# Kernel tuning notes

Hardware: AMD Instinct MI355X
Metric: run time of the kernel (lower is better)

Reference implementation:

```python
import jax, jax.numpy as jnp
import numpy as np

N, E, FDIM, HID, HEADS, C, L, G = 50000, 800000, 512, 256, 8, 32, 3, 64
EPS = 1e-5


def setup_inputs() -> dict:
    key = jax.random.key(0)
    ks = jax.random.split(key, 16)
    x = jax.random.normal(ks[0], (N, FDIM), dtype=jnp.float32)
    edge_index = jax.random.randint(ks[1], (2, E), 0, N, dtype=jnp.int32)
    batch = jnp.sort(jax.random.randint(ks[2], (N,), 0, G, dtype=jnp.int32))
    s = lambda f: 1.0 / np.sqrt(f)
    return {
        "x": x,
        "edge_index": edge_index,
        "batch": batch,
        "in_w": jax.random.normal(ks[3], (FDIM, HID), jnp.float32) * s(FDIM),
        "in_b": jnp.zeros((HID,), jnp.float32),
        "gat_w": jax.random.normal(ks[4], (L, HID, HID), jnp.float32) * s(HID),
        "att_src": jax.random.normal(ks[5], (L, HEADS, C), jnp.float32) * s(C),
        "att_dst": jax.random.normal(ks[6], (L, HEADS, C), jnp.float32) * s(C),
        "gat_b": jnp.zeros((L, HID), jnp.float32),
        "res_w": jax.random.normal(ks[7], (L, HID, HID), jnp.float32) * s(HID),
        "res_b": jnp.zeros((L, HID), jnp.float32),
        "ln_g": jnp.ones((L, HID), jnp.float32),
        "ln_b": jnp.zeros((L, HID), jnp.float32),
        "pool_w": jax.random.normal(ks[8], (2 * HID, HID), jnp.float32) * s(2 * HID),
        "pool_b": jnp.zeros((HID,), jnp.float32),
    }


def _gat_layer(h, src, dst, w, a_src, a_dst, b):
    # PyG GATConv, concat=True, negative_slope=0.2, dropout inactive (eval)
    xh = (h @ w).reshape(N, HEADS, C)                      # [N,H,C]
    asn = jnp.einsum('nhc,hc->nh', xh, a_src)              # [N,H]
    adn = jnp.einsum('nhc,hc->nh', xh, a_dst)
    e = jax.nn.leaky_relu(asn[src] + adn[dst], 0.2)        # [E2,H]
    # scatter-softmax over destination neighborhoods
    m = jax.ops.segment_max(e, dst, num_segments=N)
    m = jnp.where(jnp.isfinite(m), m, 0.0)
    ex = jnp.exp(e - m[dst])
    den = jax.ops.segment_sum(ex, dst, num_segments=N)
    alpha = ex / (den[dst] + 1e-16)                        # [E2,H]
    msg = xh[src] * alpha[:, :, None]                      # [E2,H,C]
    out = jax.ops.segment_sum(msg, dst, num_segments=N)    # [N,H,C]
    return out.reshape(N, HID) + b


def _layer_norm(h, g, b):
    mu = jnp.mean(h, axis=-1, keepdims=True)
    var = jnp.mean((h - mu) ** 2, axis=-1, keepdims=True)
    return (h - mu) * jax.lax.rsqrt(var + EPS) * g + b


def reference(x, edge_index, batch, in_w, in_b, gat_w, att_src, att_dst, gat_b,
              res_w, res_b, ln_g, ln_b, pool_w, pool_b):
    loops = jnp.arange(N, dtype=edge_index.dtype)          # GATConv add_self_loops=True
    src = jnp.concatenate([edge_index[0], loops])
    dst = jnp.concatenate([edge_index[1], loops])
    h = x @ in_w + in_b
    for i in range(L):
        h_res = h @ res_w[i] + res_b[i]
        h = _gat_layer(h, src, dst, gat_w[i], att_src[i], att_dst[i], gat_b[i])
        h = jax.nn.relu(_layer_norm(h + h_res, ln_g[i], ln_b[i]))
    ones = jnp.ones((N,), h.dtype)
    cnt = jax.ops.segment_sum(ones, batch, num_segments=G)
    h_mean = jax.ops.segment_sum(h, batch, num_segments=G) / jnp.maximum(cnt, 1.0)[:, None]
    h_max = jax.ops.segment_max(h, batch, num_segments=G)
    h_cat = jnp.concatenate([h_mean, h_max], axis=1)       # [G, 2*HID]
    return jax.nn.relu(h_cat @ pool_w + pool_b)            # [G, HID]
```

## Files before the change

kernel.cpp:

```cpp
#include <hip/hip_runtime.h>
#include <math.h>

#define N_NODES 50000
#define E_EDGES 800000
#define E2 (E_EDGES + N_NODES)
#define M_PAD 50048
#define FDIM 512
#define HID 256
#define HEADS 8
#define CDIM 32
#define LAYERS 3
#define GRAPHS 64
#define LN_EPS 1e-5f
#define POOL_P 16

typedef unsigned short ushort_t;
typedef __attribute__((ext_vector_type(8))) short short8v;
typedef __attribute__((ext_vector_type(4))) float f32x4;

__device__ __forceinline__ float bf2f(ushort_t u) {
    union { unsigned int i; float f; } v;
    v.i = ((unsigned int)u) << 16;
    return v.f;
}
__device__ __forceinline__ ushort_t f2bf(float f) {
    union { float f; unsigned int u; } v;
    v.f = f;
    unsigned int r = (v.u + 0x7FFFu + ((v.u >> 16) & 1u)) >> 16;
    return (ushort_t)r;
}
__device__ __forceinline__ void gload_lds16(const void* g, void* l) {
    __builtin_amdgcn_global_load_lds(
        (const __attribute__((address_space(1))) void*)g,
        (__attribute__((address_space(3))) void*)l, 16, 0, 0);
}

__global__ void k_count(const int* __restrict__ ei, int* __restrict__ cnt) {
    int e = blockIdx.x * 256 + threadIdx.x;
    if (e >= E2) return;
    int dst = (e < E_EDGES) ? ei[E_EDGES + e] : (e - E_EDGES);
    atomicAdd(&cnt[dst], 1);
}

__global__ void k_scan1(const int* __restrict__ cnt, int* __restrict__ part) {
    __shared__ int s[256];
    int t = threadIdx.x;
    int i = blockIdx.x * 256 + t;
    s[t] = (i < N_NODES) ? cnt[i] : 0;
    __syncthreads();
    for (int d = 128; d > 0; d >>= 1) {
        if (t < d) s[t] += s[t + d];
        __syncthreads();
    }
    if (t == 0) part[blockIdx.x] = s[0];
}

__global__ void k_scan2(int* __restrict__ part, int nb, int* __restrict__ rowptr) {
    __shared__ int s[256];
    int t = threadIdx.x;
    int v = (t < nb) ? part[t] : 0;
    s[t] = v;
    __syncthreads();
    for (int d = 1; d < 256; d <<= 1) {
        int x = (t >= d) ? s[t - d] : 0;
        __syncthreads();
        s[t] += x;
        __syncthreads();
    }
    if (t < nb) part[t] = s[t] - v;
    if (t == 255) rowptr[N_NODES] = s[255];
}

__global__ void k_scan3(const int* __restrict__ cnt, const int* __restrict__ part,
                        int* __restrict__ rowptr) {
    __shared__ int s[256];
    int t = threadIdx.x;
    int i = blockIdx.x * 256 + t;
    int v = (i < N_NODES) ? cnt[i] : 0;
    s[t] = v;
    __syncthreads();
    for (int d = 1; d < 256; d <<= 1) {
        int x = (t >= d) ? s[t - d] : 0;
        __syncthreads();
        s[t] += x;
        __syncthreads();
    }
    if (i < N_NODES) rowptr[i] = part[blockIdx.x] + s[t] - v;
}

__global__ void k_fill(const int* __restrict__ ei, const int* __restrict__ rowptr,
                       int* __restrict__ fill, int* __restrict__ colv) {
    int e = blockIdx.x * 256 + threadIdx.x;
    if (e >= E2) return;
    int src, dst;
    if (e < E_EDGES) { src = ei[e]; dst = ei[E_EDGES + e]; }
    else             { src = dst = e - E_EDGES; }
    int pos = atomicAdd(&fill[dst], 1);
    colv[rowptr[dst] + pos] = src;
}

__global__ void k_bounds(const int* __restrict__ batch, int* __restrict__ rowstart) {
    int n = blockIdx.x * 256 + threadIdx.x;
    if (n >= N_NODES) return;
    int b = batch[n];
    int bp = (n == 0) ? -1 : batch[n - 1];
    for (int g = bp + 1; g <= b; ++g) rowstart[g] = n;
    if (n == N_NODES - 1) {
        for (int g = b + 1; g <= GRAPHS; ++g) rowstart[g] = N_NODES;
    }
}

__global__ __launch_bounds__(256) void k_cast_x(const float* __restrict__ x,
                                                ushort_t* __restrict__ xb) {
    long long i8 = ((long long)blockIdx.x * 256 + threadIdx.x) * 8;
    if (i8 >= (long long)M_PAD * FDIM) return;
    int row = (int)(i8 >> 9);
    ushort_t o[8];
    if (row < N_NODES) {
        const float* p = x + i8;
        #pragma unroll
        for (int j = 0; j < 8; ++j) o[j] = f2bf(p[j]);
    } else {
        #pragma unroll
        for (int j = 0; j < 8; ++j) o[j] = 0;
    }
    *(short8v*)(xb + i8) = *(short8v*)o;
}

#define IN_ELEMS (FDIM * HID)
#define MAT_ELEMS (HID * HID)
#define WT_TOTAL (2 * LAYERS * MAT_ELEMS)
__global__ __launch_bounds__(256) void k_wtrans_all(const float* __restrict__ gat_w,
                                                    const float* __restrict__ res_w,
                                                    ushort_t* __restrict__ wt2) {
    int r = blockIdx.x * 256 + threadIdx.x;
    if (r >= WT_TOTAL) return;
    int mat = r >> 16;
    int layer = mat >> 1;
    int isgat = mat & 1;
    int within = r & 65535;
    int k = within >> 8, n = within & 255;
    const float* W = (isgat ? gat_w : res_w) + (size_t)layer * MAT_ELEMS;
    wt2[(size_t)layer * 512 * HID + (size_t)(isgat * 256 + n) * HID + k] =
        f2bf(W[within]);
}

__global__ __launch_bounds__(256) void k_wcomb(const float* __restrict__ in_w,
                                               const ushort_t* __restrict__ wt2_0,
                                               ushort_t* __restrict__ wtC) {
    __shared__ float wrow[HID];
    int n = blockIdx.x;
    wrow[threadIdx.x] = bf2f(wt2_0[(size_t)n * HID + threadIdx.x]);
    __syncthreads();
    #pragma unroll
    for (int h = 0; h < 2; ++h) {
        int f = h * 256 + threadIdx.x;
        const float* irow = in_w + (size_t)f * HID;
        float s = 0.f;
        #pragma unroll 4
        for (int k = 0; k < HID; k += 4) {
            float4 iv = *(const float4*)(irow + k);
            s += iv.x * wrow[k] + iv.y * wrow[k + 1]
               + iv.z * wrow[k + 2] + iv.w * wrow[k + 3];
        }
        wtC[(size_t)n * FDIM + f] = f2bf(s);
    }
}

__global__ __launch_bounds__(256) void k_bcomb(const float* __restrict__ in_b,
                                               const float* __restrict__ res_w0,
                                               const float* __restrict__ gat_w0,
                                               const float* __restrict__ res_b0,
                                               float* __restrict__ bC0,
                                               float* __restrict__ bC1) {
    int n = threadIdx.x;
    float s0 = 0.f, s1 = 0.f;
    for (int k = 0; k < HID; ++k) {
        float ib = in_b[k];
        s0 += ib * res_w0[(size_t)k * HID + n];
        s1 += ib * gat_w0[(size_t)k * HID + n];
    }
    bC0[n] = s0 + res_b0[n];
    bC1[n] = s1;
}

template<int K>
__global__ __launch_bounds__(256) void k_gemm_bf16(const ushort_t* __restrict__ A,
                                                   const ushort_t* __restrict__ BT,
                                                   const float* __restrict__ bias0,
                                                   const float* __restrict__ bias1,
                                                   ushort_t* __restrict__ C0,
                                                   ushort_t* __restrict__ C1,
                                                   const float* __restrict__ a_src,
                                                   const float* __restrict__ a_dst,
                                                   float* __restrict__ asn,
                                                   float* __restrict__ adn, int M) {
    __shared__ char lds[16384] __attribute__((aligned(16)));
    const int bm = blockIdx.x * 128;
    const int bn = blockIdx.y * 128;
    const int t = threadIdx.x, w = t >> 6, l = t & 63;
    const int wr = w >> 1, wc = w & 1;

    const int c1 = t, c2 = t + 256;
    const int ar1 = c1 >> 2, as1 = (c1 & 3) ^ ((ar1 >> 1) & 3);
    const int ar2 = c2 >> 2, as2 = (c2 & 3) ^ ((ar2 >> 1) & 3);
    const ushort_t* pa1 = A + (size_t)(bm + ar1) * K + as1 * 8;
    const ushort_t* pa2 = A + (size_t)(bm + ar2) * K + as2 * 8;
    const ushort_t* pb1 = BT + (size_t)(bn + ar1) * K + as1 * 8;
    const ushort_t* pb2 = BT + (size_t)(bn + ar2) * K + as2 * 8;
    char* la1 = lds + w * 1024;
    char* la2 = lds + 4096 + w * 1024;
    char* lb1 = lds + 8192 + w * 1024;
    char* lb2 = lds + 12288 + w * 1024;

    int aoff[4], boff[4];
    const int kb = l >> 4;
    #pragma unroll
    for (int mi = 0; mi < 4; ++mi) {
        int r = wr * 64 + mi * 16 + (l & 15);
        aoff[mi] = r * 64 + ((kb ^ ((r >> 1) & 3)) << 4);
        int c = wc * 64 + mi * 16 + (l & 15);
        boff[mi] = 8192 + c * 64 + ((kb ^ ((c >> 1) & 3)) << 4);
    }

    f32x4 acc[4][4] = {};
    for (int k0 = 0; k0 < K; k0 += 32) {
        gload_lds16(pa1 + k0, la1);
        gload_lds16(pa2 + k0, la2);
        gload_lds16(pb1 + k0, lb1);
        gload_lds16(pb2 + k0, lb2);
        __syncthreads();
        short8v a[4], b[4];
        #pragma unroll
        for (int mi = 0; mi < 4; ++mi) a[mi] = *(const short8v*)(lds + aoff[mi]);
        #pragma unroll
        for (int ni = 0; ni < 4; ++ni) b[ni] = *(const short8v*)(lds + boff[ni]);
        #pragma unroll
        for (int mi = 0; mi < 4; ++mi)
            #pragma unroll
            for (int ni = 0; ni < 4; ++ni)
                acc[mi][ni] = __builtin_amdgcn_mfma_f32_16x16x32_bf16(
                    a[mi], b[ni], acc[mi][ni], 0, 0, 0);
        __syncthreads();
    }

    ushort_t* C = (bn < 256) ? C0 : C1;
    const float* bias = (bn < 256) ? bias0 : bias1;
    const int cb = (bn < 256) ? bn : bn - 256;
    #pragma unroll
    for (int mi = 0; mi < 4; ++mi) {
        int row = bm + wr * 64 + mi * 16 + (l >> 4) * 4;
        #pragma unroll
        for (int ni = 0; ni < 4; ++ni) {
            int col = cb + wc * 64 + ni * 16 + (l & 15);
            float bv = bias ? bias[col] : 0.f;
            #pragma unroll
            for (int r = 0; r < 4; ++r) {
                if (row + r < M)
                    C[(size_t)(row + r) * HID + col] = f2bf(acc[mi][ni][r] + bv);
            }
        }
    }

    if (asn && bn >= 256) {
        const int cbase = bn - 256;
        #pragma unroll
        for (int mi = 0; mi < 4; ++mi) {
            int row = bm + wr * 64 + mi * 16 + (l >> 4) * 4;
            #pragma unroll
            for (int p = 0; p < 2; ++p) {
                int c0 = cbase + wc * 64 + (2 * p) * 16 + (l & 15);
                int c1c = c0 + 16;
                int head = c0 >> 5;
                float b1a = bias1 ? bias1[c0] : 0.f;
                float b1b = bias1 ? bias1[c1c] : 0.f;
                float as0 = a_src[c0], as1 = a_src[c1c];
                float ad0 = a_dst[c0], ad1 = a_dst[c1c];
                float vs[4], vd[4];
                #pragma unroll
                for (int r = 0; r < 4; ++r) {
                    float x0 = acc[mi][2 * p][r] + b1a;
                    float x1 = acc[mi][2 * p + 1][r] + b1b;
                    vs[r] = x0 * as0 + x1 * as1;
                    vd[r] = x0 * ad0 + x1 * ad1;
                }
                #pragma unroll
                for (int d = 1; d < 16; d <<= 1) {
                    #pragma unroll
                    for (int r = 0; r < 4; ++r) {
                        vs[r] += __shfl_xor(vs[r], d);
                        vd[r] += __shfl_xor(vd[r], d);
                    }
                }
                if ((l & 15) == 0) {
                    #pragma unroll
                    for (int r = 0; r < 4; ++r) {
                        if (row + r < N_NODES) {
                            asn[(row + r) * HEADS + head] = vs[r];
                            adn[(row + r) * HEADS + head] = vd[r];
                        }
                    }
                }
            }
        }
    }
}

__global__ __launch_bounds__(256) void k_agg_ln(const ushort_t* __restrict__ xhb,
                                                const float* __restrict__ asn,
                                                const float* __restrict__ adn,
                                                const int* __restrict__ rowptr,
                                                const int* __restrict__ colv,
                                                const ushort_t* __restrict__ hresb,
                                                const float* __restrict__ gb,
                                                const float* __restrict__ g,
                                                const float* __restrict__ b,
                                                ushort_t* __restrict__ hb) {
    const int wave = threadIdx.x >> 6, lane = threadIdx.x & 63;
    const int n = blockIdx.x * 4 + wave;
    if (n >= N_NODES) return;
    const int half = lane >> 5;
    const int lh = lane & 31;
    const int head = lh >> 2;
    const int ch0 = lh * 8;
    const float adn_h = adn[n * HEADS + head];
    const int j0 = rowptr[n], j1 = rowptr[n + 1];

    float acc[8] = {};
    float den = 0.f;
    int base = j0;
    for (; base + 8 <= j1; base += 8) {
        int idx[4];
        #pragma unroll
        for (int q = 0; q < 4; ++q) idx[q] = colv[base + 2 * q + half];
        short8v u[4];
        #pragma unroll
        for (int q = 0; q < 4; ++q)
            u[q] = *(const short8v*)(xhb + (size_t)idx[q] * HID + ch0);
        float p[4];
        #pragma unroll
        for (int q = 0; q < 4; ++q) {
            float e = asn[idx[q] * HEADS + head] + adn_h;
            e = (e > 0.f) ? e : 0.2f * e;
            p[q] = __expf(e);
        }
        #pragma unroll
        for (int q = 0; q < 4; ++q) {
            den += p[q];
            #pragma unroll
            for (int c = 0; c < 8; ++c)
                acc[c] += p[q] * bf2f((ushort_t)u[q][c]);
        }
    }
    for (; base < j1; base += 2) {
        bool valid = (base + half) < j1;
        int s = valid ? colv[base + half] : n;
        short8v u = *(const short8v*)(xhb + (size_t)s * HID + ch0);
        float e = asn[s * HEADS + head] + adn_h;
        e = (e > 0.f) ? e : 0.2f * e;
        float p = valid ? __expf(e) : 0.f;
        den += p;
        #pragma unroll
        for (int c = 0; c < 8; ++c)
            acc[c] += p * bf2f((ushort_t)u[c]);
    }
    den += __shfl_xor(den, 32);
    #pragma unroll
    for (int c = 0; c < 8; ++c) acc[c] += __shfl_xor(acc[c], 32);

    const float inv = 1.f / (den + 1e-16f);
    short8v hr = *(const short8v*)(hresb + (size_t)n * HID + ch0);
    float4 gbA = *(const float4*)(gb + ch0);
    float4 gbB = *(const float4*)(gb + ch0 + 4);
    float v[8];
    #pragma unroll
    for (int c = 0; c < 8; ++c) {
        float gbv = (c < 4) ? ((const float*)&gbA)[c] : ((const float*)&gbB)[c - 4];
        v[c] = acc[c] * inv + bf2f((ushort_t)hr[c]) + gbv;
    }
    float s = 0.f;
    #pragma unroll
    for (int c = 0; c < 8; ++c) s += v[c];
    #pragma unroll
    for (int d = 1; d < 32; d <<= 1) s += __shfl_xor(s, d);
    const float mu = s * (1.f / HID);
    float q = 0.f;
    #pragma unroll
    for (int c = 0; c < 8; ++c) {
        v[c] -= mu;
        q += v[c] * v[c];
    }
    #pragma unroll
    for (int d = 1; d < 32; d <<= 1) q += __shfl_xor(q, d);
    const float rstd = rsqrtf(q * (1.f / HID) + LN_EPS);
    float4 gA = *(const float4*)(g + ch0);
    float4 gB = *(const float4*)(g + ch0 + 4);
    float4 bA = *(const float4*)(b + ch0);
    float4 bB = *(const float4*)(b + ch0 + 4);
    ushort_t o[8];
    #pragma unroll
    for (int c = 0; c < 8; ++c) {
        float gv = (c < 4) ? ((const float*)&gA)[c] : ((const float*)&gB)[c - 4];
        float bv = (c < 4) ? ((const float*)&bA)[c] : ((const float*)&bB)[c - 4];
        o[c] = f2bf(fmaxf(v[c] * rstd * gv + bv, 0.f));
    }
    if (half == 0)
        *(short8v*)(hb + (size_t)n * HID + ch0) = *(short8v*)o;
}

__global__ __launch_bounds__(256) void k_pool1(const ushort_t* __restrict__ hb,
                                               const int* __restrict__ rowstart,
                                               float* __restrict__ part) {
    int g = blockIdx.x, p = blockIdx.y, c = threadIdx.x;
    int s0 = rowstart[g], s1 = rowstart[g + 1];
    float sum = 0.f, mx = -INFINITY;
    for (int n = s0 + p; n < s1; n += POOL_P) {
        float v = bf2f(hb[(size_t)n * HID + c]);
        sum += v;
        mx = fmaxf(mx, v);
    }
    float* pp = part + (size_t)(g * POOL_P + p) * 512;
    pp[c] = sum;
    pp[256 + c] = mx;
}

__global__ __launch_bounds__(256) void k_pool2g(const float* __restrict__ part,
                                                const int* __restrict__ rowstart,
                                                const float* __restrict__ W,
                                                const float* __restrict__ bias,
                                                float* __restrict__ out) {
    __shared__ float hc[512];
    int g = blockIdx.x, c = threadIdx.x;
    float sum = 0.f, mx = -INFINITY;
    for (int p = 0; p < POOL_P; ++p) {
        const float* pp = part + (size_t)(g * POOL_P + p) * 512;
        sum += pp[c];
        mx = fmaxf(mx, pp[256 + c]);
    }
    float cntf = (float)(rowstart[g + 1] - rowstart[g]);
    hc[c] = sum / fmaxf(cntf, 1.f);
    hc[256 + c] = mx;
    __syncthreads();
    float acc = bias[c];
    #pragma unroll 8
    for (int k = 0; k < 2 * HID; ++k)
        acc += hc[k] * W[(size_t)k * HID + c];
    out[(size_t)g * HID + c] = fmaxf(acc, 0.f);
}

extern "C" void kernel_launch(void* const* d_in, const int* in_sizes, int n_in,
                              void* d_out, int out_size, void* d_ws, size_t ws_size,
                              hipStream_t stream) {
    const float* x       = (const float*)d_in[0];
    const int*   ei      = (const int*)d_in[1];
    const int*   batch   = (const int*)d_in[2];
    const float* in_w    = (const float*)d_in[3];
    const float* in_b    = (const float*)d_in[4];
    const float* gat_w   = (const float*)d_in[5];
    const float* att_src = (const float*)d_in[6];
    const float* att_dst = (const float*)d_in[7];
    const float* gat_b   = (const float*)d_in[8];
    const float* res_w   = (const float*)d_in[9];
    const float* res_b   = (const float*)d_in[10];
    const float* ln_g    = (const float*)d_in[11];
    const float* ln_b    = (const float*)d_in[12];
    const float* pool_w  = (const float*)d_in[13];
    const float* pool_b  = (const float*)d_in[14];
    float* out = (float*)d_out;

    char* ws = (char*)d_ws;
    size_t off = 0;
    auto alloc = [&](size_t bytes) -> char* {
        char* p = ws + off;
        off = (off + bytes + 255) & ~(size_t)255;
        return p;
    };
    ushort_t* xb    = (ushort_t*)alloc((size_t)M_PAD * FDIM * 2);
    ushort_t* hb    = (ushort_t*)alloc((size_t)M_PAD * HID * 2);
    ushort_t* xhb   = (ushort_t*)alloc((size_t)M_PAD * HID * 2);
    ushort_t* hresb = (ushort_t*)alloc((size_t)M_PAD * HID * 2);
    float* asn      = (float*)alloc((size_t)N_NODES * HEADS * 4);
    float* adn      = (float*)alloc((size_t)N_NODES * HEADS * 4);
    int*   cnt      = (int*)alloc((size_t)N_NODES * 4);
    int*   fill     = (int*)alloc((size_t)N_NODES * 4);
    int*   rowptr   = (int*)alloc((size_t)(N_NODES + 1) * 4);
    int*   colv     = (int*)alloc((size_t)E2 * 4);
    int*   part     = (int*)alloc(256 * 4);
    int*   rowstart = (int*)alloc((size_t)(GRAPHS + 1) * 4);
    ushort_t* wt2   = (ushort_t*)alloc((size_t)LAYERS * 512 * HID * 2);
    ushort_t* wtC   = (ushort_t*)alloc((size_t)512 * FDIM * 2);
    float* bC0      = (float*)alloc(HID * 4);
    float* bC1      = (float*)alloc(HID * 4);
    float* poolpart = (float*)alloc((size_t)GRAPHS * POOL_P * 512 * 4);

    hipMemsetAsync(cnt, 0, (size_t)N_NODES * 4, stream);
    hipMemsetAsync(fill, 0, (size_t)N_NODES * 4, stream);

    const int ge = (E2 + 255) / 256;
    const int nb = (N_NODES + 255) / 256;
    k_count<<<ge, 256, 0, stream>>>(ei, cnt);
    k_scan1<<<nb, 256, 0, stream>>>(cnt, part);
    k_scan2<<<1, 256, 0, stream>>>(part, nb, rowptr);
    k_scan3<<<nb, 256, 0, stream>>>(cnt, part, rowptr);
    k_fill<<<ge, 256, 0, stream>>>(ei, rowptr, fill, colv);
    k_bounds<<<nb, 256, 0, stream>>>(batch, rowstart);

    k_cast_x<<<(int)(((size_t)M_PAD * FDIM / 8 + 255) / 256), 256, 0, stream>>>(x, xb);
    k_wtrans_all<<<(WT_TOTAL + 255) / 256, 256, 0, stream>>>(gat_w, res_w, wt2);
    k_wcomb<<<512, 256, 0, stream>>>(in_w, wt2, wtC);
    k_bcomb<<<1, 256, 0, stream>>>(in_b, res_w, gat_w, res_b, bC0, bC1);

    const int nw = (N_NODES + 3) / 4;
    dim3 gg(M_PAD / 128, 4);

    k_gemm_bf16<FDIM><<<gg, 256, 0, stream>>>(xb, wtC, bC0, bC1, hresb, xhb,
                                              att_src, att_dst, asn, adn, N_NODES);
    k_agg_ln<<<nw, 256, 0, stream>>>(xhb, asn, adn, rowptr, colv, hresb,
                                     gat_b, ln_g, ln_b, hb);

    for (int i = 1; i < LAYERS; ++i) {
        k_gemm_bf16<HID><<<gg, 256, 0, stream>>>(hb, wt2 + (size_t)i * 512 * HID,
                                                 res_b + (size_t)i * HID, nullptr,
                                                 hresb, xhb,
                                                 att_src + (size_t)i * HEADS * CDIM,
                                                 att_dst + (size_t)i * HEADS * CDIM,
                                                 asn, adn, N_NODES);
        k_agg_ln<<<nw, 256, 0, stream>>>(xhb, asn, adn, rowptr, colv, hresb,
                                         gat_b + (size_t)i * HID,
                                         ln_g + (size_t)i * HID,
                                         ln_b + (size_t)i * HID, hb);
    }
    dim3 pg(GRAPHS, POOL_P);
    k_pool1<<<pg, 256, 0, stream>>>(hb, rowstart, poolpart);
    k_pool2g<<<GRAPHS, 256, 0, stream>>>(poolpart, rowstart, pool_w, pool_b, out);
}
```

Baseline: 652.3 us.

## Use 512-thread GEMM blocks with 8 waves and fold bias kernel into wcomb

The bf16 MFMA GEMM now runs 8 waves per 128x128 tile instead of 4. Each wave computes a 32x64 sub-tile, and each thread issues one A and one B global-to-LDS load per k-step instead of two of each. This halves per-wave accumulator registers and is meant to raise latency hiding and occupancy, at the cost of more barrier participants and less per-wave reuse of B fragments. The separate single-block bias-combination kernel is merged into k_wcomb as an extra block, saving one launch.

Result: faster. 584.1 us (-10.5%).

```diff
diff --git a/kernel.cpp b/kernel.cpp
--- a/kernel.cpp
+++ b/kernel.cpp
@@ -127,7 +127,6 @@
     *(short8v*)(xb + i8) = *(short8v*)o;
 }
 
-#define IN_ELEMS (FDIM * HID)
 #define MAT_ELEMS (HID * HID)
 #define WT_TOTAL (2 * LAYERS * MAT_ELEMS)
 __global__ __launch_bounds__(256) void k_wtrans_all(const float* __restrict__ gat_w,
@@ -147,7 +146,25 @@
 
 __global__ __launch_bounds__(256) void k_wcomb(const float* __restrict__ in_w,
                                                const ushort_t* __restrict__ wt2_0,
-                                               ushort_t* __restrict__ wtC) {
+                                               const float* __restrict__ in_b,
+                                               const float* __restrict__ res_w0,
+                                               const float* __restrict__ gat_w0,
+                                               const float* __restrict__ res_b0,
+                                               ushort_t* __restrict__ wtC,
+                                               float* __restrict__ bC0,
+                                               float* __restrict__ bC1) {
+    if (blockIdx.x == 512) {
+        int n = threadIdx.x;
+        float s0 = 0.f, s1 = 0.f;
+        for (int k = 0; k < HID; ++k) {
+            float ib = in_b[k];
+            s0 += ib * res_w0[(size_t)k * HID + n];
+            s1 += ib * gat_w0[(size_t)k * HID + n];
+        }
+        bC0[n] = s0 + res_b0[n];
+        bC1[n] = s1;
+        return;
+    }
     __shared__ float wrow[HID];
     int n = blockIdx.x;
     wrow[threadIdx.x] = bf2f(wt2_0[(size_t)n * HID + threadIdx.x]);
@@ -167,25 +184,8 @@
     }
 }
 
-__global__ __launch_bounds__(256) void k_bcomb(const float* __restrict__ in_b,
-                                               const float* __restrict__ res_w0,
-                                               const float* __restrict__ gat_w0,
-                                               const float* __restrict__ res_b0,
-                                               float* __restrict__ bC0,
-                                               float* __restrict__ bC1) {
-    int n = threadIdx.x;
-    float s0 = 0.f, s1 = 0.f;
-    for (int k = 0; k < HID; ++k) {
-        float ib = in_b[k];
-        s0 += ib * res_w0[(size_t)k * HID + n];
-        s1 += ib * gat_w0[(size_t)k * HID + n];
-    }
-    bC0[n] = s0 + res_b0[n];
-    bC1[n] = s1;
-}
-
 template<int K>
-__global__ __launch_bounds__(256) void k_gemm_bf16(const ushort_t* __restrict__ A,
+__global__ __launch_bounds__(512) void k_gemm_bf16(const ushort_t* __restrict__ A,
                                                    const ushort_t* __restrict__ BT,
                                                    const float* __restrict__ bias0,
                                                    const float* __restrict__ bias1,
@@ -199,44 +199,40 @@
     const int bm = blockIdx.x * 128;
     const int bn = blockIdx.y * 128;
     const int t = threadIdx.x, w = t >> 6, l = t & 63;
-    const int wr = w >> 1, wc = w & 1;
-
-    const int c1 = t, c2 = t + 256;
-    const int ar1 = c1 >> 2, as1 = (c1 & 3) ^ ((ar1 >> 1) & 3);
-    const int ar2 = c2 >> 2, as2 = (c2 & 3) ^ ((ar2 >> 1) & 3);
-    const ushort_t* pa1 = A + (size_t)(bm + ar1) * K + as1 * 8;
-    const ushort_t* pa2 = A + (size_t)(bm + ar2) * K + as2 * 8;
-    const ushort_t* pb1 = BT + (size_t)(bn + ar1) * K + as1 * 8;
-    const ushort_t* pb2 = BT + (size_t)(bn + ar2) * K + as2 * 8;
-    char* la1 = lds + w * 1024;
-    char* la2 = lds + 4096 + w * 1024;
-    char* lb1 = lds + 8192 + w * 1024;
-    char* lb2 = lds + 12288 + w * 1024;
-
-    int aoff[4], boff[4];
+    const int wr = w & 3, wc = w >> 2;
+
+    const int arow = t >> 2;
+    const int aslot = (t & 3) ^ ((arow >> 1) & 3);
+    const ushort_t* pa = A + (size_t)(bm + arow) * K + aslot * 8;
+    const ushort_t* pb = BT + (size_t)(bn + arow) * K + aslot * 8;
+    char* la = lds + w * 1024;
+    char* lb = lds + 8192 + w * 1024;
+
+    int aoff[2], boff[4];
     const int kb = l >> 4;
     #pragma unroll
-    for (int mi = 0; mi < 4; ++mi) {
-        int r = wr * 64 + mi * 16 + (l & 15);
+    for (int mi = 0; mi < 2; ++mi) {
+        int r = wr * 32 + mi * 16 + (l & 15);
         aoff[mi] = r * 64 + ((kb ^ ((r >> 1) & 3)) << 4);
-        int c = wc * 64 + mi * 16 + (l & 15);
-        boff[mi] = 8192 + c * 64 + ((kb ^ ((c >> 1) & 3)) << 4);
-    }
-
-    f32x4 acc[4][4] = {};
+    }
+    #pragma unroll
+    for (int ni = 0; ni < 4; ++ni) {
+        int c = wc * 64 + ni * 16 + (l & 15);
+        boff[ni] = 8192 + c * 64 + ((kb ^ ((c >> 1) & 3)) << 4);
+    }
+
+    f32x4 acc[2][4] = {};
     for (int k0 = 0; k0 < K; k0 += 32) {
-        gload_lds16(pa1 + k0, la1);
-        gload_lds16(pa2 + k0, la2);
-        gload_lds16(pb1 + k0, lb1);
-        gload_lds16(pb2 + k0, lb2);
-        __syncthreads();
-        short8v a[4], b[4];
-        #pragma unroll
-        for (int mi = 0; mi < 4; ++mi) a[mi] = *(const short8v*)(lds + aoff[mi]);
+        gload_lds16(pa + k0, la);
+        gload_lds16(pb + k0, lb);
+        __syncthreads();
+        short8v a[2], b[4];
+        #pragma unroll
+        for (int mi = 0; mi < 2; ++mi) a[mi] = *(const short8v*)(lds + aoff[mi]);
         #pragma unroll
         for (int ni = 0; ni < 4; ++ni) b[ni] = *(const short8v*)(lds + boff[ni]);
         #pragma unroll
-        for (int mi = 0; mi < 4; ++mi)
+        for (int mi = 0; mi < 2; ++mi)
             #pragma unroll
             for (int ni = 0; ni < 4; ++ni)
                 acc[mi][ni] = __builtin_amdgcn_mfma_f32_16x16x32_bf16(
@@ -248,8 +244,8 @@
     const float* bias = (bn < 256) ? bias0 : bias1;
     const int cb = (bn < 256) ? bn : bn - 256;
     #pragma unroll
-    for (int mi = 0; mi < 4; ++mi) {
-        int row = bm + wr * 64 + mi * 16 + (l >> 4) * 4;
+    for (int mi = 0; mi < 2; ++mi) {
+        int row = bm + wr * 32 + mi * 16 + (l >> 4) * 4;
         #pragma unroll
         for (int ni = 0; ni < 4; ++ni) {
             int col = cb + wc * 64 + ni * 16 + (l & 15);
@@ -265,8 +261,8 @@
     if (asn && bn >= 256) {
         const int cbase = bn - 256;
         #pragma unroll
-        for (int mi = 0; mi < 4; ++mi) {
-            int row = bm + wr * 64 + mi * 16 + (l >> 4) * 4;
+        for (int mi = 0; mi < 2; ++mi) {
+            int row = bm + wr * 32 + mi * 16 + (l >> 4) * 4;
             #pragma unroll
             for (int p = 0; p < 2; ++p) {
                 int c0 = cbase + wc * 64 + (2 * p) * 16 + (l & 15);
@@ -507,19 +503,19 @@
 
     k_cast_x<<<(int)(((size_t)M_PAD * FDIM / 8 + 255) / 256), 256, 0, stream>>>(x, xb);
     k_wtrans_all<<<(WT_TOTAL + 255) / 256, 256, 0, stream>>>(gat_w, res_w, wt2);
-    k_wcomb<<<512, 256, 0, stream>>>(in_w, wt2, wtC);
-    k_bcomb<<<1, 256, 0, stream>>>(in_b, res_w, gat_w, res_b, bC0, bC1);
+    k_wcomb<<<513, 256, 0, stream>>>(in_w, wt2, in_b, res_w, gat_w, res_b,
+                                     wtC, bC0, bC1);
 
     const int nw = (N_NODES + 3) / 4;
     dim3 gg(M_PAD / 128, 4);
 
-    k_gemm_bf16<FDIM><<<gg, 256, 0, stream>>>(xb, wtC, bC0, bC1, hresb, xhb,
+    k_gemm_bf16<FDIM><<<gg, 512, 0, stream>>>(xb, wtC, bC0, bC1, hresb, xhb,
                                               att_src, att_dst, asn, adn, N_NODES);
     k_agg_ln<<<nw, 256, 0, stream>>>(xhb, asn, adn, rowptr, colv, hresb,
                                      gat_b, ln_g, ln_b, hb);
 
     for (int i = 1; i < LAYERS; ++i) {
-        k_gemm_bf16<HID><<<gg, 256, 0, stream>>>(hb, wt2 + (size_t)i * 512 * HID,
+        k_gemm_bf16<HID><<<gg, 512, 0, stream>>>(hb, wt2 + (size_t)i * 512 * HID,
                                                  res_b + (size_t)i * HID, nullptr,
                                                  hresb, xhb,
                                                  att_src + (size_t)i * HEADS * CDIM,
```
